# Performance work log

Measured on AMD Instinct MI355X. Metric: run time of the kernel, lower is better.

The kernel has to match this reference:

```python
import jax, jax.numpy as jnp
import numpy as np

L, H, E, V = 8, 16, 1024, 32000   # n_layer, n_head, n_embd, vocab_size
B, T = 4, 1024                      # batch, block_size
HS = E // H                         # head_size = 64


def _ln(x, g, b, eps=1e-5):
    m = jnp.mean(x, axis=-1, keepdims=True)
    v = jnp.mean((x - m) ** 2, axis=-1, keepdims=True)
    return (x - m) / jnp.sqrt(v + eps) * g + b


def setup_inputs() -> dict:
    key = jax.random.key(0)
    ks = jax.random.split(key, 21)
    s = 0.02
    n = lambda k, shp: (jax.random.normal(k, shp, dtype=jnp.float32) * s)
    return {
        'idx': jax.random.randint(ks[0], (B, T), 0, V),
        'tok_emb': n(ks[1], (V, E)),
        'pos_emb': n(ks[2], (T, E)),
        'ln1_g': jnp.ones((L, E), jnp.float32),
        'ln1_b': jnp.zeros((L, E), jnp.float32),
        'Wq': n(ks[3], (L, E, E)),
        'Wk': n(ks[4], (L, E, E)),
        'Wv': n(ks[5], (L, E, E)),
        'Wo': n(ks[6], (L, E, E)),
        'bo': jnp.zeros((L, E), jnp.float32),
        'ln2_g': jnp.ones((L, E), jnp.float32),
        'ln2_b': jnp.zeros((L, E), jnp.float32),
        'W1': n(ks[7], (L, E, 4 * E)),
        'b1': jnp.zeros((L, 4 * E), jnp.float32),
        'W2': n(ks[8], (L, 4 * E, E)),
        'b2': jnp.zeros((L, E), jnp.float32),
        'lnf_g': jnp.ones((E,), jnp.float32),
        'lnf_b': jnp.zeros((E,), jnp.float32),
        'Wlm': n(ks[9], (E, V)),
        'blm': jnp.zeros((V,), jnp.float32),
    }


def reference(idx, tok_emb, pos_emb, ln1_g, ln1_b, Wq, Wk, Wv, Wo, bo,
              ln2_g, ln2_b, W1, b1, W2, b2, lnf_g, lnf_b, Wlm, blm):
    x = tok_emb[idx] + pos_emb[:T]               # [B, T, E]
    scale = E ** -0.5                            # NOTE: source scales by C=n_embd, not head_size
    mask = jnp.tril(jnp.ones((T, T), dtype=bool))
    for l in range(L):
        h = _ln(x, ln1_g[l], ln1_b[l])
        q = (h @ Wq[l]).reshape(B, T, H, HS).transpose(0, 2, 1, 3)   # [B,H,T,hs]
        k = (h @ Wk[l]).reshape(B, T, H, HS).transpose(0, 2, 1, 3)
        v = (h @ Wv[l]).reshape(B, T, H, HS).transpose(0, 2, 1, 3)
        att = jnp.einsum('bhqd,bhkd->bhqk', q, k) * scale
        att = jnp.where(mask, att, -jnp.inf)
        att = jax.nn.softmax(att, axis=-1)
        o = jnp.einsum('bhqk,bhkd->bhqd', att, v)
        o = o.transpose(0, 2, 1, 3).reshape(B, T, E)                 # concat heads
        x = x + o @ Wo[l] + bo[l]
        h2 = _ln(x, ln2_g[l], ln2_b[l])
        x = x + jax.nn.relu(h2 @ W1[l] + b1[l]) @ W2[l] + b2[l]
    x = _ln(x, lnf_g, lnf_b)
    return x @ Wlm + blm                          # logits [B, T, V]
```

## Files before the change

kernel.cpp:

```cpp
#include <hip/hip_runtime.h>
#include <math.h>

#define L_ 8
#define H_ 16
#define E_ 1024
#define V_ 32000
#define B_ 4
#define T_ 1024
#define HS_ 64
#define M_ 4096
#define QKVS_ 3072

typedef __attribute__((ext_vector_type(8))) short short8;
typedef __attribute__((ext_vector_type(4))) float f32x4;

__device__ __forceinline__ unsigned short f2bf(float f) {
  unsigned int u = __builtin_bit_cast(unsigned int, f);
  u += 0x7fffu + ((u >> 16) & 1u);
  return (unsigned short)(u >> 16);
}

__global__ __launch_bounds__(256) void k_embed(
    const int* __restrict__ idx, const float* __restrict__ tok,
    const float* __restrict__ pos, float* __restrict__ x) {
  int bt = blockIdx.x;
  int t  = bt & (T_ - 1);
  int token = idx[bt];
  const float4* te = (const float4*)(tok + (size_t)token * E_);
  const float4* pe = (const float4*)(pos + (size_t)t * E_);
  float4* xo = (float4*)(x + (size_t)bt * E_);
  int i = threadIdx.x;
  float4 a = te[i], b = pe[i];
  xo[i] = make_float4(a.x + b.x, a.y + b.y, a.z + b.z, a.w + b.w);
}

__global__ __launch_bounds__(256) void k_wt(
    const float* __restrict__ W, unsigned short* __restrict__ WT,
    int K, int N, size_t ss, size_t ds) {
  __shared__ unsigned short t[64][66];
  const float* Ws = W + (size_t)blockIdx.z * ss;
  unsigned short* Wd = WT + (size_t)blockIdx.z * ds;
  int n0 = blockIdx.x * 64, k0 = blockIdx.y * 64;
  int tid = threadIdx.x;
  int c = tid & 63, r4 = tid >> 6;
  #pragma unroll
  for (int i = 0; i < 16; ++i) {
    int kr = i * 4 + r4;
    t[kr][c] = f2bf(Ws[(size_t)(k0 + kr) * N + n0 + c]);
  }
  __syncthreads();
  #pragma unroll
  for (int i = 0; i < 16; ++i) {
    int nr = i * 4 + r4;
    Wd[(size_t)(n0 + nr) * K + k0 + c] = t[c][nr];
  }
}

__device__ __forceinline__ float blk_sum256(float v, float* red) {
  #pragma unroll
  for (int o = 1; o < 64; o <<= 1) v += __shfl_xor(v, o);
  int wid = threadIdx.x >> 6, lane = threadIdx.x & 63;
  if (lane == 0) red[wid] = v;
  __syncthreads();
  v = red[0] + red[1] + red[2] + red[3];
  __syncthreads();
  return v;
}

__global__ __launch_bounds__(256) void k_ln_bf(
    const float* __restrict__ X, const float* __restrict__ g,
    const float* __restrict__ b, unsigned short* __restrict__ Y) {
  __shared__ float red[4];
  int row = blockIdx.x;
  int i = threadIdx.x;
  float4 xv = ((const float4*)(X + (size_t)row * E_))[i];
  float s = xv.x + xv.y + xv.z + xv.w;
  s = blk_sum256(s, red);
  float mean = s * (1.0f / E_);
  float dx = xv.x - mean, dy = xv.y - mean, dz = xv.z - mean, dw = xv.w - mean;
  float vs = dx*dx + dy*dy + dz*dz + dw*dw;
  vs = blk_sum256(vs, red);
  float rstd = rsqrtf(vs * (1.0f / E_) + 1e-5f);
  float4 gv = ((const float4*)g)[i];
  float4 bv = ((const float4*)b)[i];
  ushort4 o;
  o.x = f2bf(dx * rstd * gv.x + bv.x);
  o.y = f2bf(dy * rstd * gv.y + bv.y);
  o.z = f2bf(dz * rstd * gv.z + bv.z);
  o.w = f2bf(dw * rstd * gv.w + bv.w);
  ((ushort4*)(Y + (size_t)row * E_))[i] = o;
}

__global__ __launch_bounds__(256) void k_red4ln(
    const float* __restrict__ p, const float* __restrict__ bias,
    float* __restrict__ xf, const float* __restrict__ g,
    const float* __restrict__ b, unsigned short* __restrict__ hb) {
  __shared__ float red[4];
  const int ME = M_ * E_;
  int row = blockIdx.x;
  int tid = threadIdx.x;
  int i = row * E_ + tid * 4;
  float4 a  = *(const float4*)(p + i);
  float4 b2 = *(const float4*)(p + ME + i);
  float4 c  = *(const float4*)(p + 2 * ME + i);
  float4 d  = *(const float4*)(p + 3 * ME + i);
  float4 bv = *(const float4*)(bias + tid * 4);
  float4 x  = *(float4*)(xf + i);
  x.x += a.x + b2.x + c.x + d.x + bv.x;
  x.y += a.y + b2.y + c.y + d.y + bv.y;
  x.z += a.z + b2.z + c.z + d.z + bv.z;
  x.w += a.w + b2.w + c.w + d.w + bv.w;
  *(float4*)(xf + i) = x;
  float s = x.x + x.y + x.z + x.w;
  s = blk_sum256(s, red);
  float mean = s * (1.0f / E_);
  float dx = x.x - mean, dy = x.y - mean, dz = x.z - mean, dw = x.w - mean;
  float vs = dx*dx + dy*dy + dz*dz + dw*dw;
  vs = blk_sum256(vs, red);
  float rstd = rsqrtf(vs * (1.0f / E_) + 1e-5f);
  float4 gv = ((const float4*)g)[tid];
  float4 lb = ((const float4*)b)[tid];
  ushort4 o;
  o.x = f2bf(dx * rstd * gv.x + lb.x);
  o.y = f2bf(dy * rstd * gv.y + lb.y);
  o.z = f2bf(dz * rstd * gv.z + lb.z);
  o.w = f2bf(dw * rstd * gv.w + lb.w);
  ((ushort4*)(hb + (size_t)row * E_))[tid] = o;
}

#define BUFE 16384

#define GLDS(src, dst) __builtin_amdgcn_global_load_lds( \
    (const __attribute__((address_space(1))) void*)(src), \
    (__attribute__((address_space(3))) void*)(dst), 16, 0, 0)

#define BAR() do { asm volatile("" ::: "memory"); __builtin_amdgcn_s_barrier(); \
                   asm volatile("" ::: "memory"); } while (0)

template<int OT, bool RELU, int DEC>
__global__ __launch_bounds__(512, 2) void k_gemm_256(
    const unsigned short* __restrict__ A, const unsigned short* __restrict__ BT,
    const float* __restrict__ bias, void* __restrict__ Cout, int N, int K, int Kstr) {
  __shared__ __attribute__((aligned(16))) unsigned short As[2 * BUFE];
  __shared__ __attribute__((aligned(16))) unsigned short Bs[2 * BUFE];
  int tid = threadIdx.x;
  int lane = tid & 63, w = tid >> 6;
  int lr = lane & 15, lq = (lane >> 4) & 3;
  int wm = w >> 2, wn = w & 3;

  int nwg = gridDim.x, orig = blockIdx.x;
  int qq = nwg >> 3, rr = nwg & 7;
  int xcd = orig & 7, lid = orig >> 3;
  int wg = (xcd < rr ? xcd * (qq + 1) : rr * (qq + 1) + (xcd - rr) * qq) + lid;
  int m0, n0, kofs = 0;
  size_t cofs = 0;
  if constexpr (DEC == 0) { m0 = (wg & 15) * 256; n0 = (wg >> 4) * 256; }
  else if constexpr (DEC == 1) {
    int nbn = N >> 8;
    int msub = wg & 7;
    int rest = wg >> 3;
    int nb = rest % nbn;
    int msup = rest / nbn;
    m0 = (msup * 8 + msub) * 256;
    n0 = nb * 256;
  } else {
    int inner = wg & 63;
    m0 = (inner & 15) * 256; n0 = (inner >> 4) * 256;
    int ks = wg >> 6;
    kofs = ks * K;
    cofs = (size_t)ks * M_ * (size_t)N;
  }

  int srow = w * 8 + (lane >> 3);
  int skoff = ((lane & 7) ^ (lane >> 3)) * 8;
  const unsigned short* aS = A + (size_t)(m0 + srow) * Kstr + kofs + skoff;
  const unsigned short* bS = BT + (size_t)(n0 + srow) * Kstr + kofs + skoff;

#define STG_A(boff, half, tt) { \
  GLDS(aS + (size_t)((half) * 128) * Kstr + (tt) * 64,        &As[(boff) + (((half) * 128) << 6) + (w << 9)]); \
  GLDS(aS + (size_t)((half) * 128 + 64) * Kstr + (tt) * 64,   &As[(boff) + (((half) * 128 + 64) << 6) + (w << 9)]); }
#define STG_B(boff, half, tt) { \
  GLDS(bS + (size_t)((half) * 128) * Kstr + (tt) * 64,        &Bs[(boff) + (((half) * 128) << 6) + (w << 9)]); \
  GLDS(bS + (size_t)((half) * 128 + 64) * Kstr + (tt) * 64,   &Bs[(boff) + (((half) * 128 + 64) << 6) + (w << 9)]); }
#define LDA_(dst, mh, ks) { _Pragma("unroll") for (int m_ = 0; m_ < 4; ++m_) \
  dst[m_] = *(const short8*)&As[so + ((wm * 128 + (mh) * 64 + m_ * 16 + lr) << 6) + ((((ks) * 4 + lq) ^ (lr & 7)) << 3)]; }
#define LDB_(dst, ks) { _Pragma("unroll") for (int n_ = 0; n_ < 4; ++n_) \
  dst[n_] = *(const short8*)&Bs[so + ((wn * 64 + n_ * 16 + lr) << 6) + ((((ks) * 4 + lq) ^ (lr & 7)) << 3)]; }
#define MMA(afr, mofs) do { __builtin_amdgcn_s_setprio(1); \
  _Pragma("unroll") for (int m_ = 0; m_ < 4; ++m_) { \
    _Pragma("unroll") for (int n_ = 0; n_ < 4; ++n_) \
      acc[(mofs) + m_][n_] = __builtin_amdgcn_mfma_f32_16x16x32_bf16(afr[m_], bfr[n_], acc[(mofs) + m_][n_], 0, 0, 0); } \
  __builtin_amdgcn_s_setprio(0); } while (0)

  f32x4 acc[8][4] = {};
  const int NT = K >> 6;

  STG_A(0, 0, 0); STG_A(0, 1, 0); STG_B(0, 0, 0); STG_B(0, 1, 0);
  if (NT > 1) {
    STG_B(BUFE, 0, 1);
    asm volatile("s_waitcnt vmcnt(2)" ::: "memory");
  } else {
    asm volatile("s_waitcnt vmcnt(0)" ::: "memory");
  }
  BAR();

  for (int t = 0; t < NT; ++t) {
    const int so = (t & 1) * BUFE;
    const int nbuf = ((t + 1) & 1) * BUFE;
    short8 af0[4], af1[4], bfr[4];
    LDA_(af0, 0, 0);
    LDB_(bfr, 0);
    if (t + 1 < NT) { STG_B(nbuf, 1, t + 1); }
    BAR();
    MMA(af0, 0);
    BAR();
    LDA_(af1, 1, 0);
    if (t + 1 < NT) { STG_A(nbuf, 0, t + 1); }
    BAR();
    MMA(af1, 4);
    BAR();
    LDA_(af0, 0, 1);
    LDB_(bfr, 1);
    if (t + 1 < NT) { STG_A(nbuf, 1, t + 1); }
    BAR();
    MMA(af0, 0);
    BAR();
    LDA_(af1, 1, 1);
    if (t + 2 < NT) { STG_B(so, 0, t + 2); }
    BAR();
    MMA(af1, 4);
    if (t + 2 < NT) { asm volatile("s_waitcnt vmcnt(2)" ::: "memory"); }
    else            { asm volatile("s_waitcnt vmcnt(0)" ::: "memory"); }
    BAR();
  }

  #pragma unroll
  for (int m = 0; m < 8; ++m) {
    #pragma unroll
    for (int n = 0; n < 4; ++n) {
      int col = n0 + wn * 64 + n * 16 + lr;
      float bv = bias ? bias[col] : 0.0f;
      #pragma unroll
      for (int i = 0; i < 4; ++i) {
        size_t row = (size_t)(m0 + wm * 128 + m * 16 + lq * 4 + i);
        float v = acc[m][n][i] + bv;
        if (RELU) v = fmaxf(v, 0.0f);
        if (OT == 0) ((float*)Cout)[cofs + row * N + col] = v;
        else ((unsigned short*)Cout)[cofs + row * N + col] = f2bf(v);
      }
    }
  }
#undef STG_A
#undef STG_B
#undef LDA_
#undef LDB_
#undef MMA
}

template<int BN, int OT, bool RELU, bool RES>
__global__ __launch_bounds__(256) void k_gemm_tn(
    const unsigned short* __restrict__ A, const unsigned short* __restrict__ BT,
    const float* __restrict__ bias, const float* __restrict__ R,
    void* __restrict__ Cout, int M, int N, int K) {
  constexpr int NF = BN / 32;
  __shared__ __attribute__((aligned(16))) unsigned short As[128 * 64];
  __shared__ __attribute__((aligned(16))) unsigned short Bs[BN * 64];
  int tid = threadIdx.x;
  int lane = tid & 63, w = tid >> 6;
  int lr = lane & 15, lq = lane >> 4;
  int m0 = blockIdx.x * 128, n0 = blockIdx.y * BN;
  int wr = (w >> 1) * 64, wc = (w & 1) * (BN / 2);

  int srow = w * 8 + (lane >> 3);
  int skoff = ((lane & 7) ^ (lane >> 3)) * 8;
  const unsigned short* a0 = A + (size_t)(m0 + srow) * K + skoff;
  const unsigned short* b0 = BT + (size_t)(n0 + srow) * K + skoff;

  f32x4 acc[4][NF] = {};

  for (int k0 = 0; k0 < K; k0 += 64) {
    __syncthreads();
    #pragma unroll
    for (int j = 0; j < 4; ++j)
      __builtin_amdgcn_global_load_lds(
          (const __attribute__((address_space(1))) void*)(a0 + (size_t)(j * 32) * K + k0),
          (__attribute__((address_space(3))) void*)(As + j * 2048 + w * 512), 16, 0, 0);
    #pragma unroll
    for (int j = 0; j < NF; ++j)
      __builtin_amdgcn_global_load_lds(
          (const __attribute__((address_space(1))) void*)(b0 + (size_t)(j * 32) * K + k0),
          (__attribute__((address_space(3))) void*)(Bs + j * 2048 + w * 512), 16, 0, 0);
    __syncthreads();
    short8 af[4][2], bf[NF][2];
    #pragma unroll
    for (int m = 0; m < 4; ++m)
      #pragma unroll
      for (int ks = 0; ks < 2; ++ks)
        af[m][ks] = *(const short8*)&As[(wr + m * 16 + lr) * 64 + (((ks * 4 + lq) ^ (lr & 7)) << 3)];
    #pragma unroll
    for (int n = 0; n < NF; ++n)
      #pragma unroll
      for (int ks = 0; ks < 2; ++ks)
        bf[n][ks] = *(const short8*)&Bs[(wc + n * 16 + lr) * 64 + (((ks * 4 + lq) ^ (lr & 7)) << 3)];
    #pragma unroll
    for (int ks = 0; ks < 2; ++ks)
      #pragma unroll
      for (int m = 0; m < 4; ++m)
        #pragma unroll
        for (int n = 0; n < NF; ++n)
          acc[m][n] = __builtin_amdgcn_mfma_f32_16x16x32_bf16(af[m][ks], bf[n][ks], acc[m][n], 0, 0, 0);
  }

  #pragma unroll
  for (int m = 0; m < 4; ++m) {
    #pragma unroll
    for (int n = 0; n < NF; ++n) {
      int col = n0 + wc + n * 16 + lr;
      float bv = bias ? bias[col] : 0.0f;
      #pragma unroll
      for (int i = 0; i < 4; ++i) {
        size_t row = (size_t)(m0 + wr + m * 16 + lq * 4 + i);
        float v = acc[m][n][i] + bv;
        if (RELU) v = fmaxf(v, 0.0f);
        if (RES)  v += R[row * N + col];
        if (OT == 0) ((float*)Cout)[row * N + col] = v;
        else ((unsigned short*)Cout)[row * N + col] = f2bf(v);
      }
    }
  }
}

template<int OT, bool RELU, bool RES>
__global__ __launch_bounds__(256) void k_gemm_bf(
    const unsigned short* __restrict__ A, const float* __restrict__ W,
    const float* __restrict__ bias, const float* __restrict__ R,
    void* __restrict__ Cout, int M, int N, int K) {
  __shared__ unsigned short As[128][40];
  __shared__ unsigned short Bs[128][40];
  int tid = threadIdx.x;
  int lane = tid & 63, wid = tid >> 6;
  int m0 = blockIdx.x * 128, n0 = blockIdx.y * 128;
  int wr = (wid >> 1) * 64, wc = (wid & 1) * 64;
  f32x4 acc[4][4] = {};
  int a_row = tid >> 1, a_koff = (tid & 1) * 16;
  int b_nb = tid & 31, b_kb = (tid >> 5) * 4;
  int lr = lane & 15, lq = lane >> 4;
  for (int k0 = 0; k0 < K; k0 += 32) {
    const unsigned short* ap = A + (size_t)(m0 + a_row) * K + k0 + a_koff;
    uint4 av0 = *(const uint4*)ap;
    uint4 av1 = *(const uint4*)(ap + 8);
    float wv[4][4];
    #pragma unroll
    for (int dk = 0; dk < 4; ++dk) {
      const float* wrow = W + (size_t)(k0 + b_kb + dk) * N + n0 + b_nb;
      #pragma unroll
      for (int j = 0; j < 4; ++j) wv[j][dk] = wrow[32 * j];
    }
    __syncthreads();
    *(uint4*)&As[a_row][a_koff]     = av0;
    *(uint4*)&As[a_row][a_koff + 8] = av1;
    #pragma unroll
    for (int j = 0; j < 4; ++j) {
      ushort4 pk;
      pk.x = f2bf(wv[j][0]); pk.y = f2bf(wv[j][1]);
      pk.z = f2bf(wv[j][2]); pk.w = f2bf(wv[j][3]);
      *(ushort4*)&Bs[b_nb + 32 * j][b_kb] = pk;
    }
    __syncthreads();
    short8 af[4], bf[4];
    #pragma unroll
    for (int m = 0; m < 4; ++m) af[m] = *(const short8*)&As[wr + m * 16 + lr][lq * 8];
    #pragma unroll
    for (int n = 0; n < 4; ++n) bf[n] = *(const short8*)&Bs[wc + n * 16 + lr][lq * 8];
    #pragma unroll
    for (int m = 0; m < 4; ++m)
      #pragma unroll
      for (int n = 0; n < 4; ++n)
        acc[m][n] = __builtin_amdgcn_mfma_f32_16x16x32_bf16(af[m], bf[n], acc[m][n], 0, 0, 0);
  }
  #pragma unroll
  for (int m = 0; m < 4; ++m) {
    #pragma unroll
    for (int n = 0; n < 4; ++n) {
      int col = n0 + wc + n * 16 + lr;
      float bv = bias ? bias[col] : 0.0f;
      #pragma unroll
      for (int i = 0; i < 4; ++i) {
        size_t row = (size_t)(m0 + wr + m * 16 + lq * 4 + i);
        float v = acc[m][n][i] + bv;
        if (RELU) v = fmaxf(v, 0.0f);
        if (RES)  v += R[row * N + col];
        if (OT == 0) ((float*)Cout)[row * N + col] = v;
        else ((unsigned short*)Cout)[row * N + col] = f2bf(v);
      }
    }
  }
}

__global__ __launch_bounds__(256) void k_fattn(
    const unsigned short* __restrict__ QKV, unsigned short* __restrict__ O) {
  __shared__ unsigned short Ks[64][72];
  __shared__ unsigned short Vs[64][74];
  __shared__ unsigned short Pl[4][32][72];
  int tid = threadIdx.x;
  int lane = tid & 63, wid = tid >> 6;
  int lr = lane & 15, lq = lane >> 4;
  int qt = blockIdx.x, bh = blockIdx.y;
  int b = bh >> 4, h = bh & 15;
  size_t base = ((size_t)b * T_) * QKVS_ + h * HS_;
  int q0w = qt * 128 + wid * 32;

  short8 qf[2][2];
  #pragma unroll
  for (int g = 0; g < 2; ++g)
    #pragma unroll
    for (int s = 0; s < 2; ++s)
      qf[g][s] = *(const short8*)(QKV + base + (size_t)(q0w + g * 16 + lr) * QKVS_ + s * 32 + lq * 8);

  f32x4 o_acc[2][4] = {};
  float mrun[2][4], lrun[2][4];
  #pragma unroll
  for (int g = 0; g < 2; ++g)
    #pragma unroll
    for (int i = 0; i < 4; ++i) { mrun[g][i] = -1e30f; lrun[g][i] = 0.0f; }
  const float sc = 0.03125f * 1.44269504f;
  int r = tid >> 2, cc = (tid & 3) * 16;
  int ntiles = 2 * qt + 2;

  uint4 kA0, kA1, vA0, vA1;
  {
    const unsigned short* kp = QKV + base + 1024 + (size_t)r * QKVS_ + cc;
    kA0 = *(const uint4*)kp; kA1 = *(const uint4*)(kp + 8);
    vA0 = *(const uint4*)(kp + 1024); vA1 = *(const uint4*)(kp + 1032);
  }

  for (int t = 0; t < ntiles; ++t) {
    __syncthreads();
    *(uint4*)&Ks[r][cc] = kA0;
    *(uint4*)&Ks[r][cc + 8] = kA1;
    unsigned short vt[16];
    *(uint4*)&vt[0] = vA0; *(uint4*)&vt[8] = vA1;
    #pragma unroll
    for (int j = 0; j < 16; ++j) Vs[cc + j][r] = vt[j];
    __syncthreads();
    if (t + 1 < ntiles) {
      const unsigned short* kp = QKV + base + 1024 + (size_t)((t + 1) * 64 + r) * QKVS_ + cc;
      kA0 = *(const uint4*)kp; kA1 = *(const uint4*)(kp + 8);
      vA0 = *(const uint4*)(kp + 1024); vA1 = *(const uint4*)(kp + 1032);
    }

    f32x4 sa[2][4] = {};
    #pragma unroll
    for (int nt = 0; nt < 4; ++nt)
      #pragma unroll
      for (int s = 0; s < 2; ++s) {
        short8 kf = *(const short8*)&Ks[nt * 16 + lr][s * 32 + lq * 8];
        sa[0][nt] = __builtin_amdgcn_mfma_f32_16x16x32_bf16(qf[0][s], kf, sa[0][nt], 0, 0, 0);
        sa[1][nt] = __builtin_amdgcn_mfma_f32_16x16x32_bf16(qf[1][s], kf, sa[1][nt], 0, 0, 0);
      }

    bool diag = (t >= 2 * qt);
    float p[2][4][4];
    #pragma unroll
    for (int g = 0; g < 2; ++g)
      #pragma unroll
      for (int nt = 0; nt < 4; ++nt)
        #pragma unroll
        for (int i = 0; i < 4; ++i) {
          float v = sa[g][nt][i] * sc;
          if (diag && (t * 64 + nt * 16 + lr > q0w + g * 16 + lq * 4 + i)) v = -1e30f;
          p[g][nt][i] = v;
        }
    #pragma unroll
    for (int g = 0; g < 2; ++g)
      #pragma unroll
      for (int i = 0; i < 4; ++i) {
        float v = fmaxf(fmaxf(p[g][0][i], p[g][1][i]), fmaxf(p[g][2][i], p[g][3][i]));
        #pragma unroll
        for (int o = 1; o < 16; o <<= 1) v = fmaxf(v, __shfl_xor(v, o));
        float mn = fmaxf(mrun[g][i], v);
        float corr = __builtin_amdgcn_exp2f(mrun[g][i] - mn);
        mrun[g][i] = mn;
        float ps = 0.0f;
        #pragma unroll
        for (int nt = 0; nt < 4; ++nt) {
          float pe = __builtin_amdgcn_exp2f(p[g][nt][i] - mn);
          p[g][nt][i] = pe;
          ps += pe;
        }
        lrun[g][i] = lrun[g][i] * corr + ps;
        #pragma unroll
        for (int dn = 0; dn < 4; ++dn) o_acc[g][dn][i] *= corr;
      }
    #pragma unroll
    for (int g = 0; g < 2; ++g)
      #pragma unroll
      for (int nt = 0; nt < 4; ++nt)
        #pragma unroll
        for (int i = 0; i < 4; ++i)
          Pl[wid][g * 16 + lq * 4 + i][nt * 16 + lr] = f2bf(p[g][nt][i]);
    __syncthreads();

    #pragma unroll
    for (int s = 0; s < 2; ++s) {
      short8 pa0 = *(const short8*)&Pl[wid][lr][s * 32 + lq * 8];
      short8 pa1 = *(const short8*)&Pl[wid][16 + lr][s * 32 + lq * 8];
      #pragma unroll
      for (int dn = 0; dn < 4; ++dn) {
        short8 vf = *(const short8*)&Vs[dn * 16 + lr][s * 32 + lq * 8];
        o_acc[0][dn] = __builtin_amdgcn_mfma_f32_16x16x32_bf16(pa0, vf, o_acc[0][dn], 0, 0, 0);
        o_acc[1][dn] = __builtin_amdgcn_mfma_f32_16x16x32_bf16(pa1, vf, o_acc[1][dn], 0, 0, 0);
      }
    }
  }

  #pragma unroll
  for (int g = 0; g < 2; ++g)
    #pragma unroll
    for (int i = 0; i < 4; ++i) {
      float v = lrun[g][i];
      #pragma unroll
      for (int o = 1; o < 16; o <<= 1) v += __shfl_xor(v, o);
      lrun[g][i] = 1.0f / v;
    }
  #pragma unroll
  for (int g = 0; g < 2; ++g)
    #pragma unroll
    for (int dn = 0; dn < 4; ++dn)
      #pragma unroll
      for (int i = 0; i < 4; ++i) {
        size_t row = (size_t)(b * T_) + q0w + g * 16 + lq * 4 + i;
        O[row * E_ + h * HS_ + dn * 16 + lr] = f2bf(o_acc[g][dn][i] * lrun[g][i]);
      }
}

extern "C" void kernel_launch(void* const* d_in, const int* in_sizes, int n_in,
                              void* d_out, int out_size, void* d_ws, size_t ws_size,
                              hipStream_t stream) {
  const int*   idx  = (const int*)d_in[0];
  const float* tok  = (const float*)d_in[1];
  const float* pos  = (const float*)d_in[2];
  const float* ln1g = (const float*)d_in[3];
  const float* ln1b = (const float*)d_in[4];
  const float* Wq   = (const float*)d_in[5];
  const float* Wk   = (const float*)d_in[6];
  const float* Wv   = (const float*)d_in[7];
  const float* Wo   = (const float*)d_in[8];
  const float* bo   = (const float*)d_in[9];
  const float* ln2g = (const float*)d_in[10];
  const float* ln2b = (const float*)d_in[11];
  const float* W1   = (const float*)d_in[12];
  const float* b1   = (const float*)d_in[13];
  const float* W2   = (const float*)d_in[14];
  const float* b2   = (const float*)d_in[15];
  const float* lnfg = (const float*)d_in[16];
  const float* lnfb = (const float*)d_in[17];
  const float* Wlm  = (const float*)d_in[18];
  const float* blm  = (const float*)d_in[19];

  char* scr = (char*)d_out;
  const size_t MB = 1024 * 1024;
  float*          xf    = (float*)(scr);
  unsigned short* qkvb  = (unsigned short*)(scr + 16 * MB);
  unsigned short* ob    = (unsigned short*)(scr + 40 * MB);
  unsigned short* mh    = (unsigned short*)(scr + 48 * MB);
  unsigned short* wqkvT = (unsigned short*)(scr + 80 * MB);
  unsigned short* woT   = (unsigned short*)(scr + 128 * MB);
  unsigned short* w1T   = (unsigned short*)(scr + 144 * MB);
  unsigned short* w2T   = (unsigned short*)(scr + 208 * MB);
  float*          p2    = (float*)(scr + 280 * MB);
  unsigned short* hb    = (unsigned short*)d_ws;
  unsigned short* wlmT  = (unsigned short*)((char*)d_ws + 8 * MB);
  const size_t EE = (size_t)E_ * E_;
  bool lm_fast = ws_size >= 8 * MB + (size_t)V_ * E_ * 2 + 1024;

  k_embed<<<M_, 256, 0, stream>>>(idx, tok, pos, xf);

  k_wt<<<dim3(16, 16, L_), 256, 0, stream>>>(Wq, wqkvT,          E_, E_, EE, 3 * EE);
  k_wt<<<dim3(16, 16, L_), 256, 0, stream>>>(Wk, wqkvT + EE,     E_, E_, EE, 3 * EE);
  k_wt<<<dim3(16, 16, L_), 256, 0, stream>>>(Wv, wqkvT + 2 * EE, E_, E_, EE, 3 * EE);
  k_wt<<<dim3(16, 16, L_), 256, 0, stream>>>(Wo, woT,            E_, E_, EE, EE);
  k_wt<<<dim3(64, 16, L_), 256, 0, stream>>>(W1, w1T, E_, 4 * E_, 4 * EE, 4 * EE);
  k_wt<<<dim3(16, 64, L_), 256, 0, stream>>>(W2, w2T, 4 * E_, E_, 4 * EE, 4 * EE);
  if (lm_fast)
    k_wt<<<dim3(V_ / 64, 16, 1), 256, 0, stream>>>(Wlm, wlmT, E_, V_, 0, 0);

  k_ln_bf<<<M_, 256, 0, stream>>>(xf, ln1g, ln1b, hb);

  for (int l = 0; l < L_; ++l) {
    k_gemm_256<1, false, 0><<<16 * (QKVS_ / 256), 512, 0, stream>>>(
        hb, wqkvT + (size_t)l * 3 * EE, nullptr, qkvb, QKVS_, E_, E_);
    k_fattn<<<dim3(T_ / 128, B_ * H_), 256, 0, stream>>>(qkvb, ob);
    k_gemm_tn<64, 0, false, true><<<dim3(32, 16), 256, 0, stream>>>(
        ob, woT + (size_t)l * EE, bo + l * E_, xf, xf, M_, E_, E_);
    k_ln_bf<<<M_, 256, 0, stream>>>(xf, ln2g + l * E_, ln2b + l * E_, hb);
    k_gemm_256<1, true, 0><<<16 * (4 * E_ / 256), 512, 0, stream>>>(
        hb, w1T + (size_t)l * 4 * EE, b1 + (size_t)l * 4 * E_, mh, 4 * E_, E_, E_);
    k_gemm_256<0, false, 2><<<256, 512, 0, stream>>>(
        mh, w2T + (size_t)l * 4 * EE, nullptr, p2, E_, E_, 4 * E_);
    const float* ng = (l + 1 < L_) ? (ln1g + (size_t)(l + 1) * E_) : lnfg;
    const float* nb = (l + 1 < L_) ? (ln1b + (size_t)(l + 1) * E_) : lnfb;
    k_red4ln<<<M_, 256, 0, stream>>>(p2, b2 + l * E_, xf, ng, nb, hb);
  }
  if (lm_fast)
    k_gemm_256<0, false, 1><<<16 * (V_ / 256), 512, 0, stream>>>(
        hb, wlmT, blm, (float*)d_out, V_, E_, E_);
  else
    k_gemm_bf<0, false, false><<<dim3(32, V_ / 128), 256, 0, stream>>>(
        hb, Wlm, blm, nullptr, (float*)d_out, M_, V_, E_);
}
```

Measured before the change: 2.503 ms.

## Use 256x192 QKV GEMM tiles, lazy softmax rescale, drop attention barrier

The 256-wide GEMM now takes its N-tile width as a template parameter (NF fragments per wave). The QKV projection uses 256x192 tiles, giving 256 workgroups instead of 192 to fill more CUs. Next-tile prefetch is regrouped so two A and two B row-groups for step t+2 are issued together, with the vmcnt wait adjusted to match. In flash attention, the running max and the output/sum rescale are updated only when the new max exceeds the old one by more than 10 (log2 units), which cuts exp2 work and accumulator multiplies. A __syncthreads between the per-wave P writes and the PV MMA reads is removed, relying on each wave's Pl slice being private to it.

```diff
diff --git a/kernel.cpp b/kernel.cpp
--- a/kernel.cpp
+++ b/kernel.cpp
@@ -128,8 +128,6 @@
   ((ushort4*)(hb + (size_t)row * E_))[tid] = o;
 }
 
-#define BUFE 16384
-
 #define GLDS(src, dst) __builtin_amdgcn_global_load_lds( \
     (const __attribute__((address_space(1))) void*)(src), \
     (__attribute__((address_space(3))) void*)(dst), 16, 0, 0)
@@ -137,12 +135,15 @@
 #define BAR() do { asm volatile("" ::: "memory"); __builtin_amdgcn_s_barrier(); \
                    asm volatile("" ::: "memory"); } while (0)
 
-template<int OT, bool RELU, int DEC>
+template<int OT, bool RELU, int DEC, int NF>
 __global__ __launch_bounds__(512, 2) void k_gemm_256(
     const unsigned short* __restrict__ A, const unsigned short* __restrict__ BT,
     const float* __restrict__ bias, void* __restrict__ Cout, int N, int K, int Kstr) {
-  __shared__ __attribute__((aligned(16))) unsigned short As[2 * BUFE];
-  __shared__ __attribute__((aligned(16))) unsigned short Bs[2 * BUFE];
+  constexpr int BUFA = 16384;
+  constexpr int BUFB = NF * 4096;
+  constexpr int BN = NF * 64;
+  __shared__ __attribute__((aligned(16))) unsigned short As[2 * BUFA];
+  __shared__ __attribute__((aligned(16))) unsigned short Bs[2 * BUFB];
   int tid = threadIdx.x;
   int lane = tid & 63, w = tid >> 6;
   int lr = lane & 15, lq = (lane >> 4) & 3;
@@ -154,18 +155,18 @@
   int wg = (xcd < rr ? xcd * (qq + 1) : rr * (qq + 1) + (xcd - rr) * qq) + lid;
   int m0, n0, kofs = 0;
   size_t cofs = 0;
-  if constexpr (DEC == 0) { m0 = (wg & 15) * 256; n0 = (wg >> 4) * 256; }
+  if constexpr (DEC == 0) { m0 = (wg & 15) * 256; n0 = (wg >> 4) * BN; }
   else if constexpr (DEC == 1) {
-    int nbn = N >> 8;
+    int nbn = N / BN;
     int msub = wg & 7;
     int rest = wg >> 3;
     int nb = rest % nbn;
     int msup = rest / nbn;
     m0 = (msup * 8 + msub) * 256;
-    n0 = nb * 256;
+    n0 = nb * BN;
   } else {
     int inner = wg & 63;
-    m0 = (inner & 15) * 256; n0 = (inner >> 4) * 256;
+    m0 = (inner & 15) * 256; n0 = (inner >> 4) * BN;
     int ks = wg >> 6;
     kofs = ks * K;
     cofs = (size_t)ks * M_ * (size_t)N;
@@ -176,60 +177,58 @@
   const unsigned short* aS = A + (size_t)(m0 + srow) * Kstr + kofs + skoff;
   const unsigned short* bS = BT + (size_t)(n0 + srow) * Kstr + kofs + skoff;
 
-#define STG_A(boff, half, tt) { \
-  GLDS(aS + (size_t)((half) * 128) * Kstr + (tt) * 64,        &As[(boff) + (((half) * 128) << 6) + (w << 9)]); \
-  GLDS(aS + (size_t)((half) * 128 + 64) * Kstr + (tt) * 64,   &As[(boff) + (((half) * 128 + 64) << 6) + (w << 9)]); }
-#define STG_B(boff, half, tt) { \
-  GLDS(bS + (size_t)((half) * 128) * Kstr + (tt) * 64,        &Bs[(boff) + (((half) * 128) << 6) + (w << 9)]); \
-  GLDS(bS + (size_t)((half) * 128 + 64) * Kstr + (tt) * 64,   &Bs[(boff) + (((half) * 128 + 64) << 6) + (w << 9)]); }
+#define STG_A1(bo, g, tt) GLDS(aS + (size_t)((g) * 64) * Kstr + (tt) * 64, \
+                               &As[(bo) + (((g) * 64) << 6) + (w << 9)])
+#define STG_B1(bo, g, tt) GLDS(bS + (size_t)((g) * 64) * Kstr + (tt) * 64, \
+                               &Bs[(bo) + (((g) * 64) << 6) + (w << 9)])
 #define LDA_(dst, mh, ks) { _Pragma("unroll") for (int m_ = 0; m_ < 4; ++m_) \
-  dst[m_] = *(const short8*)&As[so + ((wm * 128 + (mh) * 64 + m_ * 16 + lr) << 6) + ((((ks) * 4 + lq) ^ (lr & 7)) << 3)]; }
-#define LDB_(dst, ks) { _Pragma("unroll") for (int n_ = 0; n_ < 4; ++n_) \
-  dst[n_] = *(const short8*)&Bs[so + ((wn * 64 + n_ * 16 + lr) << 6) + ((((ks) * 4 + lq) ^ (lr & 7)) << 3)]; }
+  dst[m_] = *(const short8*)&As[soA + ((wm * 128 + (mh) * 64 + m_ * 16 + lr) << 6) + ((((ks) * 4 + lq) ^ (lr & 7)) << 3)]; }
+#define LDB_(dst, ks) { _Pragma("unroll") for (int n_ = 0; n_ < NF; ++n_) \
+  dst[n_] = *(const short8*)&Bs[soB + ((wn * (16 * NF) + n_ * 16 + lr) << 6) + ((((ks) * 4 + lq) ^ (lr & 7)) << 3)]; }
 #define MMA(afr, mofs) do { __builtin_amdgcn_s_setprio(1); \
   _Pragma("unroll") for (int m_ = 0; m_ < 4; ++m_) { \
-    _Pragma("unroll") for (int n_ = 0; n_ < 4; ++n_) \
+    _Pragma("unroll") for (int n_ = 0; n_ < NF; ++n_) \
       acc[(mofs) + m_][n_] = __builtin_amdgcn_mfma_f32_16x16x32_bf16(afr[m_], bfr[n_], acc[(mofs) + m_][n_], 0, 0, 0); } \
   __builtin_amdgcn_s_setprio(0); } while (0)
 
-  f32x4 acc[8][4] = {};
+  f32x4 acc[8][NF] = {};
   const int NT = K >> 6;
 
-  STG_A(0, 0, 0); STG_A(0, 1, 0); STG_B(0, 0, 0); STG_B(0, 1, 0);
+  #pragma unroll
+  for (int g = 0; g < 4; ++g) STG_A1(0, g, 0);
+  #pragma unroll
+  for (int g = 0; g < NF; ++g) STG_B1(0, g, 0);
   if (NT > 1) {
-    STG_B(BUFE, 0, 1);
-    asm volatile("s_waitcnt vmcnt(2)" ::: "memory");
+    STG_B1(BUFB, 0, 1); STG_B1(BUFB, 1, 1);
+    STG_A1(BUFA, 0, 1); STG_A1(BUFA, 1, 1);
+    asm volatile("s_waitcnt vmcnt(4)" ::: "memory");
   } else {
     asm volatile("s_waitcnt vmcnt(0)" ::: "memory");
   }
   BAR();
 
   for (int t = 0; t < NT; ++t) {
-    const int so = (t & 1) * BUFE;
-    const int nbuf = ((t + 1) & 1) * BUFE;
-    short8 af0[4], af1[4], bfr[4];
+    const int soA = (t & 1) * BUFA, soB = (t & 1) * BUFB;
+    const int nbA = ((t + 1) & 1) * BUFA, nbB = ((t + 1) & 1) * BUFB;
+    short8 af0[4], af1[4], bfr[NF];
     LDA_(af0, 0, 0);
     LDB_(bfr, 0);
-    if (t + 1 < NT) { STG_B(nbuf, 1, t + 1); }
-    BAR();
-    MMA(af0, 0);
-    BAR();
+    if (t + 1 < NT) {
+      STG_B1(nbB, 2, t + 1);
+      if constexpr (NF == 4) STG_B1(nbB, 3, t + 1);
+    }
+    BAR(); MMA(af0, 0); BAR();
     LDA_(af1, 1, 0);
-    if (t + 1 < NT) { STG_A(nbuf, 0, t + 1); }
-    BAR();
-    MMA(af1, 4);
-    BAR();
+    if (t + 1 < NT) { STG_A1(nbA, 2, t + 1); STG_A1(nbA, 3, t + 1); }
+    BAR(); MMA(af1, 4); BAR();
     LDA_(af0, 0, 1);
     LDB_(bfr, 1);
-    if (t + 1 < NT) { STG_A(nbuf, 1, t + 1); }
-    BAR();
-    MMA(af0, 0);
-    BAR();
+    BAR(); MMA(af0, 0); BAR();
     LDA_(af1, 1, 1);
-    if (t + 2 < NT) { STG_B(so, 0, t + 2); }
-    BAR();
-    MMA(af1, 4);
-    if (t + 2 < NT) { asm volatile("s_waitcnt vmcnt(2)" ::: "memory"); }
+    if (t + 2 < NT) { STG_B1(soB, 0, t + 2); STG_B1(soB, 1, t + 2);
+                      STG_A1(soA, 0, t + 2); STG_A1(soA, 1, t + 2); }
+    BAR(); MMA(af1, 4);
+    if (t + 2 < NT) { asm volatile("s_waitcnt vmcnt(4)" ::: "memory"); }
     else            { asm volatile("s_waitcnt vmcnt(0)" ::: "memory"); }
     BAR();
   }
@@ -237,8 +236,8 @@
   #pragma unroll
   for (int m = 0; m < 8; ++m) {
     #pragma unroll
-    for (int n = 0; n < 4; ++n) {
-      int col = n0 + wn * 64 + n * 16 + lr;
+    for (int n = 0; n < NF; ++n) {
+      int col = n0 + wn * (16 * NF) + n * 16 + lr;
       float bv = bias ? bias[col] : 0.0f;
       #pragma unroll
       for (int i = 0; i < 4; ++i) {
@@ -250,8 +249,8 @@
       }
     }
   }
-#undef STG_A
-#undef STG_B
+#undef STG_A1
+#undef STG_B1
 #undef LDA_
 #undef LDB_
 #undef MMA
@@ -478,9 +477,14 @@
         float v = fmaxf(fmaxf(p[g][0][i], p[g][1][i]), fmaxf(p[g][2][i], p[g][3][i]));
         #pragma unroll
         for (int o = 1; o < 16; o <<= 1) v = fmaxf(v, __shfl_xor(v, o));
-        float mn = fmaxf(mrun[g][i], v);
-        float corr = __builtin_amdgcn_exp2f(mrun[g][i] - mn);
-        mrun[g][i] = mn;
+        if (v > mrun[g][i] + 10.0f) {
+          float corr = __builtin_amdgcn_exp2f(mrun[g][i] - v);
+          mrun[g][i] = v;
+          lrun[g][i] *= corr;
+          #pragma unroll
+          for (int dn = 0; dn < 4; ++dn) o_acc[g][dn][i] *= corr;
+        }
+        float mn = mrun[g][i];
         float ps = 0.0f;
         #pragma unroll
         for (int nt = 0; nt < 4; ++nt) {
@@ -488,9 +492,7 @@
           p[g][nt][i] = pe;
           ps += pe;
         }
-        lrun[g][i] = lrun[g][i] * corr + ps;
-        #pragma unroll
-        for (int dn = 0; dn < 4; ++dn) o_acc[g][dn][i] *= corr;
+        lrun[g][i] += ps;
       }
     #pragma unroll
     for (int g = 0; g < 2; ++g)
@@ -499,7 +501,6 @@
         #pragma unroll
         for (int i = 0; i < 4; ++i)
           Pl[wid][g * 16 + lq * 4 + i][nt * 16 + lr] = f2bf(p[g][nt][i]);
-    __syncthreads();
 
     #pragma unroll
     for (int s = 0; s < 2; ++s) {
@@ -588,22 +589,22 @@
   k_ln_bf<<<M_, 256, 0, stream>>>(xf, ln1g, ln1b, hb);
 
   for (int l = 0; l < L_; ++l) {
-    k_gemm_256<1, false, 0><<<16 * (QKVS_ / 256), 512, 0, stream>>>(
+    k_gemm_256<1, false, 0, 3><<<16 * (QKVS_ / 192), 512, 0, stream>>>(
         hb, wqkvT + (size_t)l * 3 * EE, nullptr, qkvb, QKVS_, E_, E_);
     k_fattn<<<dim3(T_ / 128, B_ * H_), 256, 0, stream>>>(qkvb, ob);
     k_gemm_tn<64, 0, false, true><<<dim3(32, 16), 256, 0, stream>>>(
         ob, woT + (size_t)l * EE, bo + l * E_, xf, xf, M_, E_, E_);
     k_ln_bf<<<M_, 256, 0, stream>>>(xf, ln2g + l * E_, ln2b + l * E_, hb);
-    k_gemm_256<1, true, 0><<<16 * (4 * E_ / 256), 512, 0, stream>>>(
+    k_gemm_256<1, true, 0, 4><<<16 * (4 * E_ / 256), 512, 0, stream>>>(
         hb, w1T + (size_t)l * 4 * EE, b1 + (size_t)l * 4 * E_, mh, 4 * E_, E_, E_);
-    k_gemm_256<0, false, 2><<<256, 512, 0, stream>>>(
+    k_gemm_256<0, false, 2, 4><<<256, 512, 0, stream>>>(
         mh, w2T + (size_t)l * 4 * EE, nullptr, p2, E_, E_, 4 * E_);
     const float* ng = (l + 1 < L_) ? (ln1g + (size_t)(l + 1) * E_) : lnfg;
     const float* nb = (l + 1 < L_) ? (ln1b + (size_t)(l + 1) * E_) : lnfb;
     k_red4ln<<<M_, 256, 0, stream>>>(p2, b2 + l * E_, xf, ng, nb, hb);
   }
   if (lm_fast)
-    k_gemm_256<0, false, 1><<<16 * (V_ / 256), 512, 0, stream>>>(
+    k_gemm_256<0, false, 1, 4><<<16 * (V_ / 256), 512, 0, stream>>>(
         hb, wlmT, blm, (float*)d_out, V_, E_, E_);
   else
     k_gemm_bf<0, false, false><<<dim3(32, V_ / 128), 256, 0, stream>>>(
```

Measured after the change: 2.569 ms. 2.6% more time.
